# Kernel tuning notes

Measured on AMD Instinct MI355X. Metric: run time of the kernel, lower is better.

The kernel has to match this reference:

```python
import jax, jax.numpy as jnp
import numpy as np

B, H, W, CIN = 8, 32, 32, 64
COUT, NOUT, KH, KW = 64, 32, 3, 3


def setup_inputs() -> dict:
    key = jax.random.key(0)
    ks = jax.random.split(key, 7)
    n_flat = H * W * COUT  # conv output flattened (same padding, stride 1)
    return {
        "x": jax.random.normal(ks[0], (B, H, W, CIN), jnp.float32),
        "w_out_u": jax.random.normal(ks[1], (B, 1, n_flat, NOUT), jnp.float32) * 0.05,
        "b_out_u": jax.random.normal(ks[2], (B, 1, NOUT), jnp.float32),
        "w_out_l": jax.random.normal(ks[3], (B, 1, n_flat, NOUT), jnp.float32) * 0.05,
        "b_out_l": jax.random.normal(ks[4], (B, 1, NOUT), jnp.float32),
        "kernel": jax.random.normal(ks[5], (KH, KW, CIN, COUT), jnp.float32) * 0.1,
        "bias": jax.random.normal(ks[6], (COUT,), jnp.float32),
    }


def reference(x, w_out_u, b_out_u, w_out_l, b_out_l, kernel, bias):
    Bb, Hh, Ww, Cin = x.shape
    Cout = kernel.shape[-1]
    n_out = w_out_u.shape[-1]
    # 'same' padding, stride 1 -> conv output spatial dims equal input dims
    Ho, Wo = Hh, Ww

    # [B,1,n_flat,n_out] -> [B,n_out,Ho,Wo,Cout]
    wu = jnp.transpose(w_out_u, (0, 1, 3, 2)).reshape(Bb, n_out, Ho, Wo, Cout)
    wl = jnp.transpose(w_out_l, (0, 1, 3, 2)).reshape(Bb, n_out, Ho, Wo, Cout)

    # bias contribution: sum over spatial + channel -> [B, n_out] -> [B,1,n_out]
    b_u = jnp.sum(wu * bias, axis=(2, 3, 4))[:, None, :] + b_out_u
    b_l = jnp.sum(wl * bias, axis=(2, 3, 4))[:, None, :] + b_out_l

    # conv2d_transpose(z, kernel) == adjoint (vjp) of the forward conv.
    # Batch the per-n_out transposed convs (the K.rnn loop) into one call.
    def conv_fwd(z):  # z: [N,H,W,Cin] -> [N,Ho,Wo,Cout]
        return jax.lax.conv_general_dilated(
            z, kernel, window_strides=(1, 1), padding="SAME",
            dimension_numbers=("NHWC", "HWIO", "NHWC"))

    zeros_in = jnp.zeros((Bb * n_out, Hh, Ww, Cin), wu.dtype)
    _, vjp_fn = jax.vjp(conv_fwd, zeros_in)

    def conv_t(w):  # [B,n_out,Ho,Wo,Cout] -> [B,n_out,H,W,Cin]
        g = vjp_fn(w.reshape(Bb * n_out, Ho, Wo, Cout))[0]
        return g.reshape(Bb, n_out, Hh, Ww, Cin)

    wu_t = conv_t(wu)
    wl_t = conv_t(wl)

    n_in = Hh * Ww * Cin
    w_u_out = jnp.transpose(wu_t.reshape(Bb, 1, n_out, n_in), (0, 1, 3, 2))
    w_l_out = jnp.transpose(wl_t.reshape(Bb, 1, n_out, n_in), (0, 1, 3, 2))
    return (w_u_out, b_u, w_l_out, b_l)
```

## Files before the change

### kernel.cpp

```cpp
#include <hip/hip_runtime.h>
#include <cstdint>

typedef __attribute__((ext_vector_type(8))) short short8;
typedef __attribute__((ext_vector_type(16))) float f32x16;
typedef __attribute__((ext_vector_type(4))) unsigned int uint4v;

__device__ inline uint32_t f2bf(float f) {
    union { float f; uint32_t u; } x; x.f = f;
    return (x.u + 0x7FFF + ((x.u >> 16) & 1)) >> 16;
}
__device__ inline uint32_t fbits(float f) {
    union { float f; uint32_t u; } x; x.f = f;
    return x.u;
}
__device__ inline float bflo(uint32_t u) {
    union { uint32_t u; float f; } x; x.u = u << 16; return x.f;
}
__device__ inline float bfhi(uint32_t u) {
    union { uint32_t u; float f; } x; x.u = u & 0xFFFF0000u; return x.f;
}

__global__ __launch_bounds__(256) void k_xform(
    const float* __restrict__ wu, const float* __restrict__ wl,
    uint4v* __restrict__ X,
    const float* __restrict__ kk, uint4v* __restrict__ AF,
    const float* __restrict__ buI, const float* __restrict__ blI,
    float* __restrict__ buO, float* __restrict__ blO)
{
    int tid = blockIdx.x * 256 + threadIdx.x;

    if (tid < 512 + 4608) {
        if (tid < 256) buO[tid] = buI[tid];
        else if (tid < 512) blO[tid - 256] = blI[tid - 256];
        else {
            int a    = tid - 512;
            int al   = a & 63;
            int c    = (a >> 6) & 1;
            int kidx = (a >> 7) & 3;
            int tap  = a >> 9;
            const float* kp = kk + ((size_t)tap * 64 + c * 32 + (al & 31)) * 64
                                 + kidx * 16 + (al >> 5) * 8;
            uint4v w;
            #pragma unroll
            for (int pr = 0; pr < 4; pr++)
                w[pr] = f2bf(kp[2 * pr]) | (f2bf(kp[2 * pr + 1]) << 16);
            AF[((tap * 4 + kidx) * 2 + c) * 64 + al] = w;
        }
    }

    int l    = tid & 63;
    int kidx = (tid >> 6) & 3;
    int site = (tid >> 8) & 1023;
    int img  = tid >> 18;
    int b    = img >> 1;
    const float* src = (img & 1) ? wl : wu;
    int o = l & 31, ch = l >> 5;

    const float* p = src + ((size_t)b * 65536 + (size_t)site * 64
                            + kidx * 16 + ch * 8) * 32 + o;
    uint4v w;
    #pragma unroll
    for (int pr = 0; pr < 4; pr++) {
        float g0 = p[(2 * pr) * 32];
        float g1 = p[(2 * pr + 1) * 32];
        w[pr] = __builtin_amdgcn_perm(fbits(g1), fbits(g0), 0x07060302u);
    }
    X[tid] = w;
}

__global__ __launch_bounds__(256, 3) void k_conv(
    const uint16_t* __restrict__ X, const uint16_t* __restrict__ AF,
    const float* __restrict__ bias,
    float* __restrict__ outU, float* __restrict__ outL,
    float* __restrict__ buO, float* __restrict__ blO)
{
    int tdx  = threadIdx.x;
    int l    = tdx & 63;
    int wid  = tdx >> 6;
    int o    = l & 31;
    int ch   = l >> 5;
    int c    = wid >> 1;
    int wsel = wid & 1;

    int bid = blockIdx.x;
    int b   = bid & 7;
    int v   = bid >> 3;
    int h   = v & 31;
    int wq  = v >> 5;
    int w0  = wq * 4 + wsel * 2;

    bool sval[4] = { w0 != 0, true, true, w0 + 2 != 32 };
    const char* XB  = (const char*)X;
    const char* AFB = (const char*)AF;

    for (int UL = 0; UL < 2; UL++) {
        int img = b * 2 + UL;
        float* dst  = UL ? outL : outU;
        float* bdst = UL ? blO : buO;

        float bp = 0.f;
        f32x16 acc[2];
        acc[0] = (f32x16)0.f;
        acc[1] = (f32x16)0.f;

        for (int r = 0; r < 3; r++) {
            int hh = h + 1 - r;
            if ((unsigned)hh >= 32u) continue;

            uint4v bw[4][4];
            #pragma unroll
            for (int si = 0; si < 4; si++) {
                int ww  = w0 - 1 + si;
                int wwc = ((unsigned)ww < 32u) ? ww : 0;
                const char* ps = XB + ((size_t)(img * 1024 + hh * 32 + wwc)) * 4096
                                    + (size_t)l * 16;
                if (sval[si]) {
                    #pragma unroll
                    for (int kidx = 0; kidx < 4; kidx++)
                        bw[si][kidx] = *(const uint4v*)(ps + kidx * 1024);
                } else {
                    #pragma unroll
                    for (int kidx = 0; kidx < 4; kidx++) bw[si][kidx] = (uint4v)0u;
                }
            }

            #pragma unroll
            for (int kidx = 0; kidx < 4; kidx++) {
                short8 A[3];
                #pragma unroll
                for (int kw = 0; kw < 3; kw++)
                    A[kw] = *(const short8*)(AFB
                            + (size_t)((((r * 3 + kw) * 4 + kidx) * 2 + c) * 64 + l) * 16);

                if (r == 1 && c == 0) {
                    float4 b0 = *(const float4*)(bias + kidx * 16 + ch * 8);
                    float4 b1 = *(const float4*)(bias + kidx * 16 + ch * 8 + 4);
                    float bb[8] = {b0.x, b0.y, b0.z, b0.w, b1.x, b1.y, b1.z, b1.w};
                    #pragma unroll
                    for (int pr = 0; pr < 4; pr++) {
                        bp = fmaf(bflo(bw[1][kidx][pr]), bb[2 * pr],
                             fmaf(bfhi(bw[1][kidx][pr]), bb[2 * pr + 1], bp));
                        bp = fmaf(bflo(bw[2][kidx][pr]), bb[2 * pr],
                             fmaf(bfhi(bw[2][kidx][pr]), bb[2 * pr + 1], bp));
                    }
                }

                #pragma unroll
                for (int si = 0; si < 4; si++) {
                    short8 Bf = __builtin_bit_cast(short8, bw[si][kidx]);
                    #pragma unroll
                    for (int tw = 0; tw < 2; tw++) {
                        int kw = tw + 2 - si;
                        if (kw >= 0 && kw <= 2)
                            acc[tw] = __builtin_amdgcn_mfma_f32_32x32x16_bf16(
                                A[kw], Bf, acc[tw], 0, 0, 0);
                    }
                }
            }
        }

        bp += __shfl_xor(bp, 32);
        if (l < 32 && c == 0) atomicAdd(&bdst[b * 32 + o], bp);

        #pragma unroll
        for (int tw = 0; tw < 2; tw++) {
            int w = w0 + tw;
            float* base = dst + ((size_t)b * 65536 + (size_t)(h * 32 + w) * 64 + c * 32) * 32;
            #pragma unroll
            for (int reg = 0; reg < 16; reg++) {
                int row = (reg & 3) + 8 * (reg >> 2) + 4 * (l >> 5);
                base[row * 32 + o] = acc[tw][reg];
            }
        }
    }
}

extern "C" void kernel_launch(void* const* d_in, const int* in_sizes, int n_in,
                              void* d_out, int out_size, void* d_ws, size_t ws_size,
                              hipStream_t stream) {
    const float* wu   = (const float*)d_in[1];
    const float* buI  = (const float*)d_in[2];
    const float* wl   = (const float*)d_in[3];
    const float* blI  = (const float*)d_in[4];
    const float* kk   = (const float*)d_in[5];
    const float* bias = (const float*)d_in[6];

    float* out  = (float*)d_out;
    float* outU = out;
    float* buO  = out + 16777216;
    float* outL = out + 16777216 + 256;
    float* blO  = out + 2 * 16777216 + 256;

    uint4v* AF = (uint4v*)d_ws;
    const size_t XOFF = 131072;
    uint4v* X = (uint4v*)((char*)d_ws + XOFF);

    k_xform<<<16384, 256, 0, stream>>>(wu, wl, X, kk, AF, buI, blI, buO, blO);
    k_conv<<<2048, 256, 0, stream>>>((const uint16_t*)X, (const uint16_t*)AF, bias,
                                     outU, outL, buO, blO);
}
```

Measured before the change: 103.7 us.

## Stage conv input tiles into LDS with async global-to-LDS double buffering

Instead of each wave loading its own input sites from global memory into registers, the block cooperatively DMAs the six shared input sites for the 4-wide tile into a double-buffered LDS tile using global_load_lds. The four waves share these tiles, so the overlapping sites neighbouring waves read are fetched once, and the next kernel row's load is issued before computing the current one. This aims to cut redundant global traffic and hide load latency. In exchange it adds 48KB of LDS per block, which may limit occupancy against the launch bound of 3 blocks, plus block-wide barriers.

```diff
diff --git a/kernel.cpp b/kernel.cpp
--- a/kernel.cpp
+++ b/kernel.cpp
@@ -18,6 +18,12 @@
 }
 __device__ inline float bfhi(uint32_t u) {
     union { uint32_t u; float f; } x; x.u = u & 0xFFFF0000u; return x.f;
+}
+
+__device__ inline void dma16(const void* g, void* lds) {
+    __builtin_amdgcn_global_load_lds(
+        (const __attribute__((address_space(1))) unsigned int*)g,
+        (__attribute__((address_space(3))) unsigned int*)lds, 16, 0, 0);
 }
 
 __global__ __launch_bounds__(256) void k_xform(
@@ -74,6 +80,8 @@
     float* __restrict__ outU, float* __restrict__ outL,
     float* __restrict__ buO, float* __restrict__ blO)
 {
+    __shared__ uint16_t tiles[2][6][4][512];
+
     int tdx  = threadIdx.x;
     int l    = tdx & 63;
     int wid  = tdx >> 6;
@@ -89,7 +97,9 @@
     int wq  = v >> 5;
     int w0  = wq * 4 + wsel * 2;
 
-    bool sval[4] = { w0 != 0, true, true, w0 + 2 != 32 };
+    int rstart = (h == 31) ? 1 : 0;
+    int nr     = (h == 0 || h == 31) ? 2 : 3;
+
     const char* XB  = (const char*)X;
     const char* AFB = (const char*)AF;
 
@@ -103,27 +113,25 @@
         acc[0] = (f32x16)0.f;
         acc[1] = (f32x16)0.f;
 
-        for (int r = 0; r < 3; r++) {
+        auto STAGE = [&](int bf, int r) {
             int hh = h + 1 - r;
-            if ((unsigned)hh >= 32u) continue;
-
-            uint4v bw[4][4];
-            #pragma unroll
-            for (int si = 0; si < 4; si++) {
-                int ww  = w0 - 1 + si;
-                int wwc = ((unsigned)ww < 32u) ? ww : 0;
-                const char* ps = XB + ((size_t)(img * 1024 + hh * 32 + wwc)) * 4096
-                                    + (size_t)l * 16;
-                if (sval[si]) {
-                    #pragma unroll
-                    for (int kidx = 0; kidx < 4; kidx++)
-                        bw[si][kidx] = *(const uint4v*)(ps + kidx * 1024);
+            #pragma unroll
+            for (int i = 0; i < 6; i++) {
+                int p = wid * 6 + i;
+                int s = p >> 2, k = p & 3;
+                int ww = wq * 4 - 1 + s;
+                void* ldst = (void*)&tiles[bf][s][k][0];
+                if ((unsigned)ww < 32u) {
+                    const char* g = XB + ((size_t)(img * 1024 + hh * 32 + ww)) * 4096
+                                       + (size_t)k * 1024 + (size_t)l * 16;
+                    dma16(g, ldst);
                 } else {
-                    #pragma unroll
-                    for (int kidx = 0; kidx < 4; kidx++) bw[si][kidx] = (uint4v)0u;
+                    *(uint4v*)((char*)ldst + l * 16) = (uint4v)0u;
                 }
             }
-
+        };
+
+        auto COMPUTE = [&](int bf, int r) {
             #pragma unroll
             for (int kidx = 0; kidx < 4; kidx++) {
                 short8 A[3];
@@ -132,22 +140,29 @@
                     A[kw] = *(const short8*)(AFB
                             + (size_t)((((r * 3 + kw) * 4 + kidx) * 2 + c) * 64 + l) * 16);
 
+                uint4v bw[4];
+                #pragma unroll
+                for (int si = 0; si < 4; si++) {
+                    int s = 2 * wsel + si;
+                    bw[si] = *(const uint4v*)((const char*)&tiles[bf][s][kidx][0] + l * 16);
+                }
+
                 if (r == 1 && c == 0) {
                     float4 b0 = *(const float4*)(bias + kidx * 16 + ch * 8);
                     float4 b1 = *(const float4*)(bias + kidx * 16 + ch * 8 + 4);
                     float bb[8] = {b0.x, b0.y, b0.z, b0.w, b1.x, b1.y, b1.z, b1.w};
                     #pragma unroll
                     for (int pr = 0; pr < 4; pr++) {
-                        bp = fmaf(bflo(bw[1][kidx][pr]), bb[2 * pr],
-                             fmaf(bfhi(bw[1][kidx][pr]), bb[2 * pr + 1], bp));
-                        bp = fmaf(bflo(bw[2][kidx][pr]), bb[2 * pr],
-                             fmaf(bfhi(bw[2][kidx][pr]), bb[2 * pr + 1], bp));
+                        bp = fmaf(bflo(bw[1][pr]), bb[2 * pr],
+                             fmaf(bfhi(bw[1][pr]), bb[2 * pr + 1], bp));
+                        bp = fmaf(bflo(bw[2][pr]), bb[2 * pr],
+                             fmaf(bfhi(bw[2][pr]), bb[2 * pr + 1], bp));
                     }
                 }
 
                 #pragma unroll
                 for (int si = 0; si < 4; si++) {
-                    short8 Bf = __builtin_bit_cast(short8, bw[si][kidx]);
+                    short8 Bf = __builtin_bit_cast(short8, bw[si]);
                     #pragma unroll
                     for (int tw = 0; tw < 2; tw++) {
                         int kw = tw + 2 - si;
@@ -157,6 +172,15 @@
                     }
                 }
             }
+        };
+
+        STAGE(0, rstart);
+        __syncthreads();
+        for (int i = 0; i < nr; i++) {
+            int r = rstart + i;
+            if (i + 1 < nr) STAGE((i + 1) & 1, r + 1);
+            COMPUTE(i & 1, r);
+            __syncthreads();
         }
 
         bp += __shfl_xor(bp, 32);
```

After: 102.4 us. About the same (-1.2%).
